# Optimization experiments

Measured on AMD Instinct MI355X. Metric: run time of the kernel, lower is better.

The kernel has to match this reference:

```python
import jax, jax.numpy as jnp
import numpy as np

HEAD_DIM = 64
NUM_HEADS = 32
ROPE_THETA = 10000.0


def _rope_cos_sin(seq_len, dim, theta, dtype):
    inv_freq = 1.0 / (theta ** (jnp.arange(0, dim, 2, dtype=jnp.float32) / dim))
    t = jnp.arange(seq_len, dtype=jnp.float32)
    freqs = jnp.outer(t, inv_freq)  # [T, dim/2]
    return jnp.cos(freqs).astype(dtype), jnp.sin(freqs).astype(dtype)


def _apply_rope(x, cos, sin):
    # x: [B, T, H, D]; GPT-NeoX style (split halves), matching flash-attn rotary (interleaved=False)
    d2 = x.shape[-1] // 2
    x1, x2 = x[..., :d2], x[..., d2:]
    c = cos[None, :, None, :]
    s = sin[None, :, None, :]
    return jnp.concatenate([x1 * c - x2 * s, x2 * c + x1 * s], axis=-1)


def setup_inputs() -> dict:
    key = jax.random.key(0)
    ks = jax.random.split(key, 8)
    B, T, Dm = 2, 2048, 2048
    H, Dh = NUM_HEADS, HEAD_DIM
    sc = 1.0 / np.sqrt(Dm)
    return {
        "hidden_states": jax.random.normal(ks[0], (B, T, Dm), jnp.float32),
        "v1": jax.random.normal(ks[1], (B, T, H, Dh), jnp.float32),
        "lambda1": jax.random.uniform(ks[2], (), jnp.float32),
        "Wq": jax.random.normal(ks[3], (Dm, Dm), jnp.float32) * sc,
        "Wk": jax.random.normal(ks[4], (Dm, Dm), jnp.float32) * sc,
        "Wv": jax.random.normal(ks[5], (Dm, Dm), jnp.float32) * sc,
        "Wo": jax.random.normal(ks[6], (Dm, Dm), jnp.float32) * sc,
        "lambda2": jnp.float32(0.5),
    }


def reference(hidden_states, v1, lambda1, Wq, Wk, Wv, Wo, lambda2):
    B, T, Dm = hidden_states.shape
    H, Dh = NUM_HEADS, HEAD_DIM
    # QKV projections + head split
    q = (hidden_states @ Wq).reshape(B, T, H, Dh)
    k = (hidden_states @ Wk).reshape(B, T, H, Dh)
    v = (hidden_states @ Wv).reshape(B, T, H, Dh)
    # Value residual mixing: V' = lambda1 * V_1 + lambda2 * V_n
    v = lambda1 * v1 + lambda2 * v
    # RoPE (seqlen_offset = 0, no cache)
    cos, sin = _rope_cos_sin(T, Dh, ROPE_THETA, q.dtype)
    q = _apply_rope(q, cos, sin)
    k = _apply_rope(k, cos, sin)
    # Causal attention (flash_attn_func(..., causal=True) equivalent)
    scale = 1.0 / np.sqrt(Dh)
    scores = jnp.einsum("bqhd,bkhd->bhqk", q, k) * scale
    causal = jnp.tril(jnp.ones((T, T), dtype=bool))
    scores = jnp.where(causal[None, None], scores, jnp.finfo(scores.dtype).min)
    probs = jax.nn.softmax(scores, axis=-1)
    o = jnp.einsum("bhqk,bkhd->bqhd", probs, v).reshape(B, T, Dm)
    return o @ Wo
```

## Files before the change

kernel.cpp:

```cpp
#include <hip/hip_runtime.h>
#include <hip/hip_bf16.h>
#include <math.h>

typedef __bf16 bf16;
typedef __bf16 bf16x8 __attribute__((ext_vector_type(8)));
typedef __bf16 bf16x4 __attribute__((ext_vector_type(4)));
typedef float  f32x4  __attribute__((ext_vector_type(4)));
typedef short  sv4    __attribute__((ext_vector_type(4)));

#define B_  2
#define T_  2048
#define DM  2048
#define H_  32
#define DH  64

__device__ __forceinline__ bf16x8 load8(const bf16* p) {
    return *reinterpret_cast<const bf16x8*>(p);
}

__device__ __forceinline__ void gld16(const bf16* g, bf16* l) {
    __builtin_amdgcn_global_load_lds(
        (const __attribute__((address_space(1))) unsigned int*)g,
        (__attribute__((address_space(3))) unsigned int*)l, 16, 0, 0);
}

__global__ void k_convert(const float* __restrict__ in, bf16* __restrict__ out, int n4) {
    int i = blockIdx.x * blockDim.x + threadIdx.x;
    if (i < n4) {
        float4 v = reinterpret_cast<const float4*>(in)[i];
        bf16x4 o;
        o[0] = (bf16)v.x; o[1] = (bf16)v.y; o[2] = (bf16)v.z; o[3] = (bf16)v.w;
        reinterpret_cast<bf16x4*>(out)[i] = o;
    }
}

__global__ void k_transposeW(const float* __restrict__ Wq, const float* __restrict__ Wk,
                             const float* __restrict__ Wv, const float* __restrict__ Wo,
                             bf16* __restrict__ WqT, bf16* __restrict__ WkT,
                             bf16* __restrict__ WvT, bf16* __restrict__ WoT) {
    const float* in; bf16* out;
    switch (blockIdx.z) {
        case 0: in = Wq; out = WqT; break;
        case 1: in = Wk; out = WkT; break;
        case 2: in = Wv; out = WvT; break;
        default: in = Wo; out = WoT; break;
    }
    __shared__ float tile[32][33];
    int tx = threadIdx.x, ty = threadIdx.y;
    int x0 = blockIdx.x * 32, y0 = blockIdx.y * 32;
    #pragma unroll
    for (int i = 0; i < 4; i++)
        tile[ty + i*8][tx] = in[(size_t)(y0 + ty + i*8) * DM + x0 + tx];
    __syncthreads();
    #pragma unroll
    for (int i = 0; i < 4; i++)
        out[(size_t)(x0 + ty + i*8) * DM + y0 + tx] = (bf16)tile[tx][ty + i*8];
}

template<int OUT_BF16>
__global__ __launch_bounds__(256)
void k_gemm(const bf16* __restrict__ A, const bf16* __restrict__ BT,
            void* __restrict__ Cout, int ldc) {
    constexpr int K = 2048;
    __shared__ bf16 ldsA[128 * 32];
    __shared__ bf16 ldsB[128 * 32];
    int tid = threadIdx.x;
    int lane = tid & 63, w = tid >> 6;
    int l16 = lane & 15, quad = lane >> 4;
    int wm = w >> 1, wn = w & 1;
    int mblk = blockIdx.y * 128, nblk = blockIdx.x * 128;

    f32x4 acc[4][4] = {};

    int sgz = ((lane & 3) ^ ((lane >> 3) & 3)) * 8;
    const bf16* gA = A  + (size_t)(mblk + w * 32 + (lane >> 2)) * K + sgz;
    const bf16* gB = BT + (size_t)(nblk + w * 32 + (lane >> 2)) * K + sgz;
    bf16* lA = ldsA + w * 1024;
    bf16* lB = ldsB + w * 1024;
    int sA = (quad ^ ((l16 >> 1) & 3)) * 8;

    for (int k0 = 0; k0 < K; k0 += 32) {
        gld16(gA + k0,          lA);
        gld16(gA + 16 * K + k0, lA + 512);
        gld16(gB + k0,          lB);
        gld16(gB + 16 * K + k0, lB + 512);
        __syncthreads();
        bf16x8 af[4], bfr[4];
        #pragma unroll
        for (int s = 0; s < 4; s++)
            af[s] = *reinterpret_cast<bf16x8*>(&ldsA[(wm * 64 + s * 16 + l16) * 32 + sA]);
        #pragma unroll
        for (int t = 0; t < 4; t++)
            bfr[t] = *reinterpret_cast<bf16x8*>(&ldsB[(wn * 64 + t * 16 + l16) * 32 + sA]);
        #pragma unroll
        for (int s = 0; s < 4; s++)
            #pragma unroll
            for (int t = 0; t < 4; t++)
                acc[s][t] = __builtin_amdgcn_mfma_f32_16x16x32_bf16(af[s], bfr[t], acc[s][t], 0, 0, 0);
        __syncthreads();
    }

    #pragma unroll
    for (int s = 0; s < 4; s++) {
        int row = mblk + wm * 64 + s * 16 + quad * 4;
        #pragma unroll
        for (int t = 0; t < 4; t++) {
            int col = nblk + wn * 64 + t * 16 + l16;
            #pragma unroll
            for (int r = 0; r < 4; r++) {
                if (OUT_BF16)
                    reinterpret_cast<bf16*>(Cout)[(size_t)(row + r) * ldc + col] = (bf16)acc[s][t][r];
                else
                    reinterpret_cast<float*>(Cout)[(size_t)(row + r) * ldc + col] = acc[s][t][r];
            }
        }
    }
}

template<int OUT_BF16>
__global__ __launch_bounds__(512, 2)
void k_gemm256(const bf16* __restrict__ A, const bf16* __restrict__ BT,
               void* __restrict__ Cout, int ldc) {
    constexpr int K = 2048;
    __shared__ bf16 lds[32768];
    const int tid  = threadIdx.x;
    const int lane = tid & 63, w = tid >> 6;
    const int l16  = lane & 15, quad = lane >> 4;
    const int wm   = w >> 2, wn = w & 3;
    const size_t mblk = (size_t)blockIdx.y * 256, nblk = (size_t)blockIdx.x * 256;

    f32x4 acc[8][4] = {};

    const int sg = (((tid & 3) ^ ((tid >> 3) & 3)) << 3);
    const bf16* gA = A  + (mblk + (tid >> 2)) * K + sg;
    const bf16* gB = BT + (nblk + (tid >> 2)) * K + sg;

    const int segr = ((quad ^ ((l16 >> 1) & 3)) << 3);
    const int aoff = (wm * 128 + l16) * 32 + segr;
    const int boff = (wn * 64  + l16) * 32 + segr;

#define STGA(kt_) do { \
    const bf16* g_ = gA + (kt_) * 32; \
    bf16* l_ = lds + ((((kt_) & 1) << 14) + 8192) + w * 512; \
    gld16(g_, l_); gld16(g_ + 128 * 2048, l_ + 4096); \
} while (0)

#define STGB(kt_) do { \
    const bf16* g_ = gB + (kt_) * 32; \
    bf16* l_ = lds + (((kt_) & 1) << 14) + w * 512; \
    gld16(g_, l_); gld16(g_ + 128 * 2048, l_ + 4096); \
} while (0)

#define LD4(dst_, i0_, base_) do { \
    _Pragma("unroll") for (int i_ = 0; i_ < 4; ++i_) \
        dst_[(i0_) + i_] = *reinterpret_cast<const bf16x8*>((base_) + i_ * 512); \
} while (0)

#define MFMA16(mh_) do { \
    _Pragma("unroll") for (int mi_ = 0; mi_ < 4; ++mi_) \
        _Pragma("unroll") for (int ni_ = 0; ni_ < 4; ++ni_) \
            acc[(mh_) * 4 + mi_][ni_] = __builtin_amdgcn_mfma_f32_16x16x32_bf16( \
                af[(mh_) * 4 + mi_], bq[ni_], acc[(mh_) * 4 + mi_][ni_], 0, 0, 0); \
} while (0)

#define BAR  __builtin_amdgcn_s_barrier()
#define PRI1 __builtin_amdgcn_s_setprio(1)
#define PRI0 __builtin_amdgcn_s_setprio(0)
#define LGK0 asm volatile("s_waitcnt lgkmcnt(0)" ::: "memory")
#define VM4  asm volatile("s_waitcnt vmcnt(4)" ::: "memory")
#define VM0  asm volatile("s_waitcnt vmcnt(0)" ::: "memory")

#define TILE(cb_, SA_, SB_, VM_) do { \
    const bf16* rb_ = lds + (cb_) + boff; \
    const bf16* ra_ = lds + (cb_) + 8192 + aoff; \
    bf16x8 af[8], bq[4]; \
    LD4(af, 0, ra_); \
    LD4(af, 4, ra_ + 2048); \
    LD4(bq, 0, rb_); \
    LGK0; \
    BAR; \
    SA_; \
    PRI1; MFMA16(0); PRI0; \
    SB_; \
    PRI1; MFMA16(1); PRI0; \
    VM_; \
    BAR; \
} while (0)

    STGB(0); STGA(0); STGB(1); STGA(1);
    VM4;
    BAR;

    #pragma unroll 1
    for (int t = 0; t < 61; t += 2) {
        TILE(0,     STGA(t + 2), STGB(t + 2), VM4);
        TILE(16384, STGA(t + 3), STGB(t + 3), VM4);
    }
    TILE(0,     (void)0, (void)0, VM0);
    TILE(16384, (void)0, (void)0, (void)0);

#undef STGA
#undef STGB
#undef LD4
#undef MFMA16
#undef BAR
#undef PRI1
#undef PRI0
#undef LGK0
#undef VM4
#undef VM0
#undef TILE

    #pragma unroll
    for (int mt = 0; mt < 8; ++mt) {
        size_t row = mblk + wm * 128 + mt * 16 + quad * 4;
        #pragma unroll
        for (int nt = 0; nt < 4; ++nt) {
            size_t col = nblk + wn * 64 + nt * 16 + l16;
            #pragma unroll
            for (int r = 0; r < 4; ++r) {
                if (OUT_BF16)
                    reinterpret_cast<bf16*>(Cout)[(row + r) * (size_t)ldc + col] = (bf16)acc[mt][nt][r];
                else
                    reinterpret_cast<float*>(Cout)[(row + r) * (size_t)ldc + col] = acc[mt][nt][r];
            }
        }
    }
}

__global__ void k_tab(float2* __restrict__ tab) {
    int id = blockIdx.x * 256 + threadIdx.x;
    int i = id & 31, t = id >> 5;
    float inv = __builtin_amdgcn_exp2f(-(float)i * 0.41524101186092037f);
    float ang = (float)t * inv;
    float s, c;
    __sincosf(ang, &s, &c);
    tab[id] = make_float2(c, s);
}

__global__ void k_rope(bf16* __restrict__ qkv, const float2* __restrict__ tab) {
    int id = blockIdx.x * 256 + threadIdx.x;
    int j   = id & 3;
    int h   = (id >> 2) & 31;
    int sel = (id >> 7) & 1;
    int t   = (id >> 8) & 2047;
    int b   = id >> 19;
    size_t base = ((size_t)(b * T_ + t)) * 6144 + sel * 2048 + h * 64 + j * 8;
    bf16x8 x1 = load8(qkv + base);
    bf16x8 x2 = load8(qkv + base + 32);
    const float2* tp = tab + t * 32 + j * 8;
    bf16x8 o1, o2;
    #pragma unroll
    for (int e = 0; e < 8; e++) {
        float c = tp[e].x, s = tp[e].y;
        float a = (float)x1[e], v = (float)x2[e];
        o1[e] = (bf16)(a * c - v * s);
        o2[e] = (bf16)(v * c + a * s);
    }
    *reinterpret_cast<bf16x8*>(qkv + base)      = o1;
    *reinterpret_cast<bf16x8*>(qkv + base + 32) = o2;
}

__global__ void k_combinev(const float* __restrict__ v1, const bf16* __restrict__ qkv,
                           const float* __restrict__ l1p, const float* __restrict__ l2p,
                           bf16* __restrict__ vT) {
    __shared__ float tile[64 * 33];
    float l1 = l1p[0], l2 = l2p[0];
    int b = blockIdx.y >> 5, h = blockIdx.y & 31;
    int t0 = blockIdx.x * 32;
    int tid = threadIdx.x;
    int d = tid & 63, tr = tid >> 6;
    #pragma unroll
    for (int i = 0; i < 8; i++) {
        int t = t0 + i * 4 + tr;
        size_t iv1 = ((size_t)(b * T_ + t)) * 2048 + h * 64 + d;
        size_t ivg = ((size_t)(b * T_ + t)) * 6144 + 4096 + h * 64 + d;
        tile[d * 33 + i * 4 + tr] = l1 * v1[iv1] + l2 * (float)qkv[ivg];
    }
    __syncthreads();
    int tl = tid & 31, dr = tid >> 5;
    #pragma unroll
    for (int j = 0; j < 8; j++) {
        int d2 = dr + j * 8;
        vT[((size_t)((b * H_ + h) * 64 + d2)) * T_ + t0 + tl] = (bf16)tile[d2 * 33 + tl];
    }
}

__global__ __launch_bounds__(256)
void k_attn(const bf16* __restrict__ qkv, const bf16* __restrict__ vT, bf16* __restrict__ o) {
    __shared__ bf16 ldsK[64 * 64];
    __shared__ bf16 ldsV[64 * 64];
    int bx = blockIdx.x;
    int bh = blockIdx.y;
    int b = bh >> 5, h = bh & 31;
    int tid = threadIdx.x;
    int lane = tid & 63, w = tid >> 6;
    int l16 = lane & 15, quad = lane >> 4;

    int rl = lane >> 3, sg = ((lane & 7) ^ rl) * 8;
    const bf16* kgl = qkv + ((size_t)(b * T_) + w * 16 + rl) * 6144 + 2048 + h * 64 + sg;
    const bf16* vgl = vT + ((size_t)bh * DH + w * 16 + rl) * T_ + sg;
    bf16* lKw = ldsK + w * 16 * 64;
    bf16* lVw = ldsV + w * 16 * 64;

    int skey = (quad ^ (l16 & 7)) * 8;
    int skey2 = ((quad + 4) ^ (l16 & 7)) * 8;

    #pragma unroll 1
    for (int pass = 0; pass < 2; pass++) {
        int qt = pass ? (31 - bx) : bx;
        int qbase = qt * 64 + w * 16;

        size_t qrow = (size_t)(b * T_ + qbase + l16) * 6144 + h * 64;
        bf16x8 qf[2];
        #pragma unroll
        for (int half = 0; half < 2; half++) {
            bf16x8 v = load8(qkv + qrow + half * 32 + quad * 8);
            #pragma unroll
            for (int e = 0; e < 8; e++) v[e] = (bf16)((float)v[e] * 0.1803368801f);
            qf[half] = v;
        }

        f32x4 accO[4] = {};
        float m_ = -1e30f, pl = 0.f;

        int nkt = qt + 1;
        for (int kt = 0; kt < nkt; kt++) {
            int key0 = kt * 64;
            #pragma unroll
            for (int j = 0; j < 2; j++) {
                gld16(kgl + (size_t)(key0 + j * 8) * 6144, lKw + j * 512);
                gld16(vgl + (size_t)(j * 8) * T_ + key0,   lVw + j * 512);
            }
            __syncthreads();

            bool diag = (kt == qt);
            f32x4 st[4];
            sv4 pk[4];
            #pragma unroll
            for (int ks = 0; ks < 4; ks++) {
                if (!diag || key0 + ks * 16 <= qbase + 15) {
                    bf16x8 kf0 = *reinterpret_cast<bf16x8*>(&ldsK[(ks * 16 + l16) * 64 + skey]);
                    bf16x8 kf1 = *reinterpret_cast<bf16x8*>(&ldsK[(ks * 16 + l16) * 64 + skey2]);
                    f32x4 z = {};
                    z = __builtin_amdgcn_mfma_f32_16x16x32_bf16(kf0, qf[0], z, 0, 0, 0);
                    z = __builtin_amdgcn_mfma_f32_16x16x32_bf16(kf1, qf[1], z, 0, 0, 0);
                    st[ks] = z;
                } else {
                    st[ks] = (f32x4){-3e38f, -3e38f, -3e38f, -3e38f};
                }
            }

            if (diag) {
                int qcol = qbase + l16;
                #pragma unroll
                for (int ks = 0; ks < 4; ks++)
                    #pragma unroll
                    for (int r = 0; r < 4; r++)
                        if (key0 + ks * 16 + quad * 4 + r > qcol) st[ks][r] = -3e38f;
            }

            float mx = st[0][0];
            #pragma unroll
            for (int ks = 0; ks < 4; ks++)
                #pragma unroll
                for (int r = 0; r < 4; r++) mx = fmaxf(mx, st[ks][r]);
            mx = fmaxf(mx, __shfl_xor(mx, 16));
            mx = fmaxf(mx, __shfl_xor(mx, 32));
            if (__any(mx > m_)) {
                float nm = fmaxf(m_, mx);
                float alpha = __builtin_amdgcn_exp2f(m_ - nm);
                m_ = nm;
                pl *= alpha;
                #pragma unroll
                for (int n2 = 0; n2 < 4; n2++) accO[n2] *= alpha;
            }
            float rsum = 0.f;
            #pragma unroll
            for (int ks = 0; ks < 4; ks++) {
                bf16x4 ph;
                #pragma unroll
                for (int r = 0; r < 4; r++) {
                    float p = __builtin_amdgcn_exp2f(st[ks][r] - m_);
                    rsum += p;
                    ph[r] = (bf16)p;
                }
                pk[ks] = __builtin_bit_cast(sv4, ph);
            }
            pl += rsum;

            #pragma unroll
            for (int ks = 0; ks < 4; ks++) {
                if (!diag || key0 + ks * 16 <= qbase + 15) {
                    int svf = ((ks * 2 + (quad >> 1)) ^ (l16 & 7)) * 8 + (quad & 1) * 4;
                    #pragma unroll
                    for (int n2 = 0; n2 < 4; n2++) {
                        sv4 vf = *reinterpret_cast<sv4*>(&ldsV[(n2 * 16 + l16) * 64 + svf]);
                        accO[n2] = __builtin_amdgcn_mfma_f32_16x16x16bf16_1k(
                            vf, pk[ks], accO[n2], 0, 0, 0);
                    }
                }
            }
            __syncthreads();
        }

        float l = pl;
        l += __shfl_xor(l, 16);
        l += __shfl_xor(l, 32);
        float inv = 1.0f / l;
        int query = qbase + l16;
        #pragma unroll
        for (int n2 = 0; n2 < 4; n2++) {
            bf16x4 ov;
            #pragma unroll
            for (int r = 0; r < 4; r++) ov[r] = (bf16)(accO[n2][r] * inv);
            *reinterpret_cast<bf16x4*>(
                &o[(size_t)(b * T_ + query) * DM + h * 64 + n2 * 16 + quad * 4]) = ov;
        }
    }
}

extern "C" void kernel_launch(void* const* d_in, const int* in_sizes, int n_in,
                              void* d_out, int out_size, void* d_ws, size_t ws_size,
                              hipStream_t stream) {
    const float* hs   = (const float*)d_in[0];
    const float* v1   = (const float*)d_in[1];
    const float* lam1 = (const float*)d_in[2];
    const float* Wq   = (const float*)d_in[3];
    const float* Wk   = (const float*)d_in[4];
    const float* Wv   = (const float*)d_in[5];
    const float* Wo   = (const float*)d_in[6];
    const float* lam2 = (const float*)d_in[7];

    char* ws = (char*)d_ws;
    bf16* hs_bf = (bf16*)(ws);
    float2* tab = (float2*)(ws);
    bf16* Wcat  = (bf16*)(ws + 16777216);
    bf16* WoT   = (bf16*)(ws + 41943040);
    bf16* qkv   = (bf16*)(ws + 50331648);
    bf16* vT_bf = (bf16*)(ws + 100663296);
    bf16* o_bf  = (bf16*)(ws + 117440512);

    k_convert<<<8192, 256, 0, stream>>>(hs, hs_bf, 2097152);
    k_transposeW<<<dim3(64, 64, 4), dim3(32, 8), 0, stream>>>(
        Wq, Wk, Wv, Wo, Wcat, Wcat + 4194304, Wcat + 8388608, WoT);

    k_gemm256<1><<<dim3(24, 16), 512, 0, stream>>>(hs_bf, Wcat, (void*)qkv, 6144);

    k_tab<<<256, 256, 0, stream>>>(tab);
    k_rope<<<4096, 256, 0, stream>>>(qkv, tab);

    k_combinev<<<dim3(64, 64), 256, 0, stream>>>(v1, qkv, lam1, lam2, vT_bf);

    k_attn<<<dim3(16, 64), 256, 0, stream>>>(qkv, vT_bf, o_bf);

    k_gemm<0><<<dim3(16, 32), 256, 0, stream>>>(o_bf, WoT, d_out, 2048);
}
```

Baseline: 440.0 us.

## Triple-buffer QKV GEMM LDS stages with dynamic shared memory

Converts the 256x256 QKV GEMM from a double-buffered to a triple-buffered LDS pipeline, using 96KB of dynamic shared memory set via a function attribute. Each tile now loads all A/B fragments, issues the next-next stage's global->LDS copies, waits, barriers once, then runs all 32 MFMAs in one burst instead of splitting MFMAs around two staged load groups. The aim is to hide more global-load latency and cut one barrier per tile. In exchange the larger LDS footprint likely allows only one 512-thread block per CU, against launch bounds asking for two. That turns the 384-block grid into more than one wave, and it also drops the earlier in-tile interleaving of loads and MFMAs.

Result: faster. 430.3 us (-2.2%).

```diff
diff --git a/kernel.cpp b/kernel.cpp
--- a/kernel.cpp
+++ b/kernel.cpp
@@ -122,7 +122,7 @@
 void k_gemm256(const bf16* __restrict__ A, const bf16* __restrict__ BT,
                void* __restrict__ Cout, int ldc) {
     constexpr int K = 2048;
-    __shared__ bf16 lds[32768];
+    extern __shared__ bf16 lds[];
     const int tid  = threadIdx.x;
     const int lane = tid & 63, w = tid >> 6;
     const int l16  = lane & 15, quad = lane >> 4;
@@ -139,74 +139,59 @@
     const int aoff = (wm * 128 + l16) * 32 + segr;
     const int boff = (wn * 64  + l16) * 32 + segr;
 
-#define STGA(kt_) do { \
-    const bf16* g_ = gA + (kt_) * 32; \
-    bf16* l_ = lds + ((((kt_) & 1) << 14) + 8192) + w * 512; \
-    gld16(g_, l_); gld16(g_ + 128 * 2048, l_ + 4096); \
-} while (0)
-
-#define STGB(kt_) do { \
-    const bf16* g_ = gB + (kt_) * 32; \
-    bf16* l_ = lds + (((kt_) & 1) << 14) + w * 512; \
-    gld16(g_, l_); gld16(g_ + 128 * 2048, l_ + 4096); \
-} while (0)
-
-#define LD4(dst_, i0_, base_) do { \
-    _Pragma("unroll") for (int i_ = 0; i_ < 4; ++i_) \
-        dst_[(i0_) + i_] = *reinterpret_cast<const bf16x8*>((base_) + i_ * 512); \
-} while (0)
-
-#define MFMA16(mh_) do { \
-    _Pragma("unroll") for (int mi_ = 0; mi_ < 4; ++mi_) \
-        _Pragma("unroll") for (int ni_ = 0; ni_ < 4; ++ni_) \
-            acc[(mh_) * 4 + mi_][ni_] = __builtin_amdgcn_mfma_f32_16x16x32_bf16( \
-                af[(mh_) * 4 + mi_], bq[ni_], acc[(mh_) * 4 + mi_][ni_], 0, 0, 0); \
+#define STG(kt_, buf_) do { \
+    const bf16* ga_ = gA + (kt_) * 32; \
+    const bf16* gb_ = gB + (kt_) * 32; \
+    bf16* lb_ = lds + (buf_) * 16384 + w * 512; \
+    bf16* la_ = lds + (buf_) * 16384 + 8192 + w * 512; \
+    gld16(gb_, lb_); gld16(gb_ + 128 * 2048, lb_ + 4096); \
+    gld16(ga_, la_); gld16(ga_ + 128 * 2048, la_ + 4096); \
 } while (0)
 
 #define BAR  __builtin_amdgcn_s_barrier()
 #define PRI1 __builtin_amdgcn_s_setprio(1)
 #define PRI0 __builtin_amdgcn_s_setprio(0)
-#define LGK0 asm volatile("s_waitcnt lgkmcnt(0)" ::: "memory")
 #define VM4  asm volatile("s_waitcnt vmcnt(4)" ::: "memory")
 #define VM0  asm volatile("s_waitcnt vmcnt(0)" ::: "memory")
 
-#define TILE(cb_, SA_, SB_, VM_) do { \
+#define TILE(cb_, SG_, VM_) do { \
     const bf16* rb_ = lds + (cb_) + boff; \
     const bf16* ra_ = lds + (cb_) + 8192 + aoff; \
     bf16x8 af[8], bq[4]; \
-    LD4(af, 0, ra_); \
-    LD4(af, 4, ra_ + 2048); \
-    LD4(bq, 0, rb_); \
-    LGK0; \
-    BAR; \
-    SA_; \
-    PRI1; MFMA16(0); PRI0; \
-    SB_; \
-    PRI1; MFMA16(1); PRI0; \
+    _Pragma("unroll") for (int i_ = 0; i_ < 8; ++i_) \
+        af[i_] = *reinterpret_cast<const bf16x8*>(ra_ + i_ * 512); \
+    _Pragma("unroll") for (int i_ = 0; i_ < 4; ++i_) \
+        bq[i_] = *reinterpret_cast<const bf16x8*>(rb_ + i_ * 512); \
+    SG_; \
     VM_; \
     BAR; \
+    PRI1; \
+    _Pragma("unroll") for (int mi_ = 0; mi_ < 8; ++mi_) \
+        _Pragma("unroll") for (int ni_ = 0; ni_ < 4; ++ni_) \
+            acc[mi_][ni_] = __builtin_amdgcn_mfma_f32_16x16x32_bf16( \
+                af[mi_], bq[ni_], acc[mi_][ni_], 0, 0, 0); \
+    PRI0; \
 } while (0)
 
-    STGB(0); STGA(0); STGB(1); STGA(1);
+    STG(0, 0); STG(1, 1);
     VM4;
     BAR;
 
     #pragma unroll 1
-    for (int t = 0; t < 61; t += 2) {
-        TILE(0,     STGA(t + 2), STGB(t + 2), VM4);
-        TILE(16384, STGA(t + 3), STGB(t + 3), VM4);
-    }
-    TILE(0,     (void)0, (void)0, VM0);
-    TILE(16384, (void)0, (void)0, (void)0);
-
-#undef STGA
-#undef STGB
-#undef LD4
-#undef MFMA16
+    for (int t = 0; t < 60; t += 3) {
+        TILE(0,     STG(t + 2, 2), VM4);
+        TILE(16384, STG(t + 3, 0), VM4);
+        TILE(32768, STG(t + 4, 1), VM4);
+    }
+    TILE(0,     STG(62, 2), VM4);
+    TILE(16384, STG(63, 0), VM4);
+    TILE(32768, (void)0,    VM0);
+    TILE(0,     (void)0,    (void)0);
+
+#undef STG
 #undef BAR
 #undef PRI1
 #undef PRI0
-#undef LGK0
 #undef VM4
 #undef VM0
 #undef TILE
@@ -226,6 +211,17 @@
             }
         }
     }
+}
+
+namespace {
+struct GemmLdsInit {
+    GemmLdsInit() {
+        (void)hipFuncSetAttribute(
+            reinterpret_cast<const void*>(&k_gemm256<1>),
+            hipFuncAttributeMaxDynamicSharedMemorySize, 98304);
+    }
+};
+GemmLdsInit g_ldsInit;
 }
 
 __global__ void k_tab(float2* __restrict__ tab) {
@@ -445,7 +441,7 @@
     k_transposeW<<<dim3(64, 64, 4), dim3(32, 8), 0, stream>>>(
         Wq, Wk, Wv, Wo, Wcat, Wcat + 4194304, Wcat + 8388608, WoT);
 
-    k_gemm256<1><<<dim3(24, 16), 512, 0, stream>>>(hs_bf, Wcat, (void*)qkv, 6144);
+    k_gemm256<1><<<dim3(24, 16), 512, 98304, stream>>>(hs_bf, Wcat, (void*)qkv, 6144);
 
     k_tab<<<256, 256, 0, stream>>>(tab);
     k_rope<<<4096, 256, 0, stream>>>(qkv, tab);
```
